# Performance work log

Measured on AMD Instinct MI355X. Metric: run time of the kernel, lower is better.

The kernel has to match this reference:

```python
import jax, jax.numpy as jnp
import numpy as np

N_IMG, BATCH, SEQ, D_IN, H = 32, 1024, 64, 16, 16


def setup_inputs() -> dict:
    key = jax.random.key(0)
    k1, k2, k3, k4, k5 = jax.random.split(key, 5)
    s = 1.0 / np.sqrt(H)  # torch nn.LSTM default init: U(-1/sqrt(H), 1/sqrt(H))
    return {
        "images": jax.random.normal(k1, (N_IMG, BATCH, SEQ, D_IN), jnp.float32),
        "w_ih": jax.random.uniform(k2, (4 * H, D_IN), jnp.float32, -s, s),
        "w_hh": jax.random.uniform(k3, (4 * H, H), jnp.float32, -s, s),
        "b_ih": jax.random.uniform(k4, (4 * H,), jnp.float32, -s, s),
        "b_hh": jax.random.uniform(k5, (4 * H,), jnp.float32, -s, s),
    }


def reference(images, w_ih, w_hh, b_ih, b_hh):
    # images: [N, B, S, D]. The torch module loops over N chunks, feeding each
    # [B, S, D] chunk through nn.LSTM while carrying (h, c) across chunks.
    # Equivalent: one continuous recurrence over N*S timesteps.
    n, b, s, d = images.shape
    h_dim = w_hh.shape[1]
    # time-major: [N*S, B, D]
    xs = images.transpose(0, 2, 1, 3).reshape(n * s, b, d)
    # precompute input projections for all timesteps (the only big GEMM)
    x_proj = jnp.einsum('tbd,gd->tbg', xs, w_ih) + (b_ih + b_hh)  # [T, B, 4H]

    def cell(carry, xp_t):
        h_prev, c_prev = carry
        gates = xp_t + h_prev @ w_hh.T  # [B, 4H]; torch gate order: i, f, g, o
        i, f, g, o = jnp.split(gates, 4, axis=-1)
        c = jax.nn.sigmoid(f) * c_prev + jax.nn.sigmoid(i) * jnp.tanh(g)
        h_new = jax.nn.sigmoid(o) * jnp.tanh(c)
        return (h_new, c), h_new

    h0 = jnp.zeros((b, h_dim), images.dtype)
    (_, _), outs = jax.lax.scan(cell, (h0, h0), x_proj)  # outs: [T, B, H]
    # torch stacks per-chunk outputs [B, S, H] along dim 0 -> [N, B, S, H]
    return outs.reshape(n, s, b, h_dim).transpose(0, 2, 1, 3)
```

## Files before the change

kernel.cpp:

```cpp
#include <hip/hip_runtime.h>

#define LOG2E      1.44269504088896340736f
#define TWO_LOG2E  2.88539008177792680472f

typedef float f2 __attribute__((ext_vector_type(2)));

__device__ __forceinline__ float frcp(float x)  { return __builtin_amdgcn_rcpf(x); }
__device__ __forceinline__ float fexp2(float x) { return __builtin_amdgcn_exp2f(x); }

__device__ __forceinline__ f2 pk_mul(f2 a, f2 b) {
    f2 d; asm("v_pk_mul_f32 %0, %1, %2" : "=v"(d) : "v"(a), "v"(b)); return d;
}
__device__ __forceinline__ f2 pk_fma(f2 a, f2 b, f2 c) {
    f2 d; asm("v_pk_fma_f32 %0, %1, %2, %3" : "=v"(d) : "v"(a), "v"(b), "v"(c)); return d;
}
__device__ __forceinline__ f2 pk_add(f2 a, f2 b) {
    f2 d; asm("v_pk_add_f32 %0, %1, %2" : "=v"(d) : "v"(a), "v"(b)); return d;
}

__device__ __forceinline__ void gload_lds16(const float* g, float* l) {
    auto gp = (const __attribute__((address_space(1))) float*)g;
    auto lp = (__attribute__((address_space(3))) float*)l;
    __builtin_amdgcn_global_load_lds(gp, lp, 16, 0, 0);
}


__global__ __launch_bounds__(256, 1)
void lstm_fused(const float* __restrict__ images,
                const float* __restrict__ w_ih,
                const float* __restrict__ w_hh,
                const float* __restrict__ b_ih,
                const float* __restrict__ b_hh,
                float* __restrict__ out)
{
    __shared__ float4 xlds[4][2][256];

    const int lane = threadIdx.x & 63;
    const int wid  = threadIdx.x >> 6;
    const int b    = (blockIdx.x << 2) + wid;
    const int a    = lane >> 4;
    const int j    = lane & 15;

    int rr1 = __builtin_amdgcn_update_dpp(0, j, 0x121, 0xF, 0xF, true);
    const int d_ror = (rr1 - j) & 15;

    int e16;
    { int pa = a, pb = a;
      asm volatile("s_nop 1\n\t"
                   "v_permlane16_swap_b32 %0, %1" : "+v"(pa), "+v"(pb));
      e16 = pa & 1; }
    int e32;
    { int pc = a, pd = a;
      asm volatile("s_nop 1\n\t"
                   "v_permlane32_swap_b32 %0, %1" : "+v"(pc), "+v"(pd));
      e32 = (pc < 2) ? 0 : 1; }

    const int m1 = ((a >> 1) == e32);
    const int m0 = ((a & 1) == e16);
    const int gate = m0 ? (m1 ? 1 : 2) : (m1 ? 0 : 3);
    const int r = gate * 16 + j;

    const float aa = (gate == 2) ? TWO_LOG2E : -LOG2E;
    const float mm = (gate == 2) ? -2.0f * TWO_LOG2E : 1.0f;
    const float dd = (gate == 2) ? TWO_LOG2E : 0.0f;

    float whh[16];
#pragma unroll
    for (int t = 0; t < 16; ++t)
        whh[t] = aa * w_hh[r * 16 + ((j + d_ror * t) & 15)];
    f2 wihp[8];
#pragma unroll
    for (int m = 0; m < 8; ++m) {
        f2 w; w.x = aa * w_ih[r * 16 + 2 * m]; w.y = aa * w_ih[r * 16 + 2 * m + 1];
        wihp[m] = w;
    }
    const float bias = aa * (b_ih[r] + b_hh[r]);

    float hv = 0.0f;
    float c  = 0.0f;
    float sv = 0.0f;

    const int bbase = b << 10;

#define PB(p) ((((p) >> 4) << 20) + bbase + (((((p) << 2)) & 63) << 4))

#define GLOAD_CHUNK(n) {                                                       \
        const float* gp_ = images + ((n) << 20) + bbase + (lane << 2);         \
        float4* lb_ = &xlds[wid][(n) & 1][0];                                  \
        gload_lds16(gp_ + 0,   (float*)(lb_ + 0));                             \
        gload_lds16(gp_ + 256, (float*)(lb_ + 64));                            \
        gload_lds16(gp_ + 512, (float*)(lb_ + 128));                           \
        gload_lds16(gp_ + 768, (float*)(lb_ + 192)); }

#define DSREAD(xv2, Qraw) {                                                    \
        int Q_ = (Qraw); if (Q_ > 511) Q_ = 511;                               \
        const float4* sp_ = &xlds[wid][(Q_ >> 4) & 1][(Q_ & 15) << 4];         \
        _Pragma("unroll")                                                      \
        for (int q = 0; q < 16; ++q) {                                         \
            float4 t_ = sp_[q];                                                \
            f2 lo_, hi_; lo_.x = t_.x; lo_.y = t_.y; hi_.x = t_.z; hi_.y = t_.w;\
            xv2[2*q] = lo_; xv2[2*q+1] = hi_;                                  \
        } }

#define PROJ(xpre, x2) {                                                       \
        _Pragma("unroll")                                                      \
        for (int u = 0; u < 4; ++u) {                                          \
            f2 A_ = pk_mul(wihp[0], x2[8*u+0]);                                \
            f2 B_ = pk_mul(wihp[1], x2[8*u+1]);                                \
            A_ = pk_fma(wihp[2], x2[8*u+2], A_);                               \
            B_ = pk_fma(wihp[3], x2[8*u+3], B_);                               \
            A_ = pk_fma(wihp[4], x2[8*u+4], A_);                               \
            B_ = pk_fma(wihp[5], x2[8*u+5], B_);                               \
            A_ = pk_fma(wihp[6], x2[8*u+6], A_);                               \
            B_ = pk_fma(wihp[7], x2[8*u+7], B_);                               \
            A_ = pk_add(A_, B_);                                               \
            xpre[u] = (bias + A_.x) + A_.y;                                    \
        } }

#define STEP(u, xpv) {                                                         \
        float p0 = (xpv), p1, p2, p3;                                          \
        asm volatile(                                                          \
          "s_nop 1\n\t"                                                        \
          "v_fmac_f32 %[q0], %[h], %[w0]\n\t"                                  \
          "v_mul_f32 %[q1], %[h], %[w1] row_ror:1 row_mask:0xf bank_mask:0xf\n\t" \
          "v_mul_f32 %[q2], %[h], %[w2] row_ror:2 row_mask:0xf bank_mask:0xf\n\t" \
          "v_mul_f32 %[q3], %[h], %[w3] row_ror:3 row_mask:0xf bank_mask:0xf\n\t" \
          "v_fmac_f32 %[q0], %[h], %[w4] row_ror:4 row_mask:0xf bank_mask:0xf\n\t" \
          "v_fmac_f32 %[q1], %[h], %[w5] row_ror:5 row_mask:0xf bank_mask:0xf\n\t" \
          "v_fmac_f32 %[q2], %[h], %[w6] row_ror:6 row_mask:0xf bank_mask:0xf\n\t" \
          "v_fmac_f32 %[q3], %[h], %[w7] row_ror:7 row_mask:0xf bank_mask:0xf\n\t" \
          "v_fmac_f32 %[q0], %[h], %[w8] row_ror:8 row_mask:0xf bank_mask:0xf\n\t" \
          "v_fmac_f32 %[q1], %[h], %[w9] row_ror:9 row_mask:0xf bank_mask:0xf\n\t" \
          "v_fmac_f32 %[q2], %[h], %[w10] row_ror:10 row_mask:0xf bank_mask:0xf\n\t" \
          "v_fmac_f32 %[q3], %[h], %[w11] row_ror:11 row_mask:0xf bank_mask:0xf\n\t" \
          "v_fmac_f32 %[q0], %[h], %[w12] row_ror:12 row_mask:0xf bank_mask:0xf\n\t" \
          "v_fmac_f32 %[q1], %[h], %[w13] row_ror:13 row_mask:0xf bank_mask:0xf\n\t" \
          "v_fmac_f32 %[q2], %[h], %[w14] row_ror:14 row_mask:0xf bank_mask:0xf\n\t" \
          "v_fmac_f32 %[q3], %[h], %[w15] row_ror:15 row_mask:0xf bank_mask:0xf"   \
          : [q0]"+v"(p0), [q1]"=&v"(p1), [q2]"=&v"(p2), [q3]"=&v"(p3)          \
          : [h]"v"(hv),                                                        \
            [w0]"v"(whh[0]),  [w1]"v"(whh[1]),  [w2]"v"(whh[2]),  [w3]"v"(whh[3]), \
            [w4]"v"(whh[4]),  [w5]"v"(whh[5]),  [w6]"v"(whh[6]),  [w7]"v"(whh[7]), \
            [w8]"v"(whh[8]),  [w9]"v"(whh[9]),  [w10]"v"(whh[10]),[w11]"v"(whh[11]),\
            [w12]"v"(whh[12]),[w13]"v"(whh[13]),[w14]"v"(whh[14]),[w15]"v"(whh[15]));\
        float arg = (p0 + p1) + (p2 + p3);                                     \
        float act = fmaf(mm, frcp(1.0f + fexp2(arg)), dd);                     \
        float qf, qg, qi, qo;                                                  \
        asm volatile(                                                          \
          "v_mov_b32 %[A], %[x]\n\t"                                           \
          "v_mov_b32 %[B], %[x]\n\t"                                           \
          "s_nop 1\n\t"                                                        \
          "v_permlane16_swap_b32 %[A], %[B]\n\t"                               \
          "v_mov_b32 %[C], %[A]\n\t"                                           \
          "v_mov_b32 %[D], %[B]\n\t"                                           \
          "v_permlane32_swap_b32 %[A], %[C]\n\t"                               \
          "v_permlane32_swap_b32 %[B], %[D]"                                   \
          : [A]"=&v"(qf), [B]"=&v"(qi), [C]"=&v"(qg), [D]"=&v"(qo)             \
          : [x]"v"(act));                                                      \
        c = fmaf(c, qf, qi * qg);                                              \
        float tc = fmaf(-2.0f, frcp(1.0f + fexp2(c)), 1.0f);                   \
        hv = qo * tc;                                                          \
        sv = (a == (u)) ? hv : sv;                                             \
    }

#define STORE(pb) out[(pb) + lane] = sv;

    f2    xvA[32], xvB[32];
    float xpre[4];

    GLOAD_CHUNK(0);
    GLOAD_CHUNK(1);
    DSREAD(xvA, 0);
    PROJ(xpre, xvA);
    DSREAD(xvB, 1);

#pragma unroll 1
    for (int P = 0; P < 512; P += 2) {
        {
            const int pb = PB(P);
            STEP(0, xpre[0]);
            STEP(1, xpre[1]);
            STEP(2, xpre[2]);
            STEP(3, xpre[3]);
            STORE(pb);
        }
        PROJ(xpre, xvB);
        DSREAD(xvA, P + 2);
        if ((P & 15) == 14 && P < 480)
            GLOAD_CHUNK((P >> 4) + 2);
        {
            const int pb = PB(P + 1);
            STEP(0, xpre[0]);
            STEP(1, xpre[1]);
            STEP(2, xpre[2]);
            STEP(3, xpre[3]);
            STORE(pb);
        }
        PROJ(xpre, xvA);
        DSREAD(xvB, P + 3);
    }

#undef STEP
#undef STORE
#undef PROJ
#undef DSREAD
#undef GLOAD_CHUNK
#undef PB
}

extern "C" void kernel_launch(void* const* d_in, const int* in_sizes, int n_in,
                              void* d_out, int out_size, void* d_ws, size_t ws_size,
                              hipStream_t stream)
{
    const float* images = (const float*)d_in[0];
    const float* w_ih   = (const float*)d_in[1];
    const float* w_hh   = (const float*)d_in[2];
    const float* b_ih   = (const float*)d_in[3];
    const float* b_hh   = (const float*)d_in[4];
    float* outp         = (float*)d_out;

    lstm_fused<<<dim3(256), dim3(256), 0, stream>>>(images, w_ih, w_hh, b_ih, b_hh, outp);
}
```

Baseline: 324.1 us.

## Hand-schedule LDS reads with explicit waitcnt and shorten the tanh chain

Result: faster. 292.6 us (-9.7%).

```diff
diff --git a/kernel.cpp b/kernel.cpp
--- a/kernel.cpp
+++ b/kernel.cpp
@@ -17,6 +17,8 @@
 __device__ __forceinline__ f2 pk_add(f2 a, f2 b) {
     f2 d; asm("v_pk_add_f32 %0, %1, %2" : "=v"(d) : "v"(a), "v"(b)); return d;
 }
+__device__ __forceinline__ f2 f2lo(float4 v) { f2 r; r.x = v.x; r.y = v.y; return r; }
+__device__ __forceinline__ f2 f2hi(float4 v) { f2 r; r.x = v.z; r.y = v.w; return r; }
 
 __device__ __forceinline__ void gload_lds16(const float* g, float* l) {
     auto gp = (const __attribute__((address_space(1))) float*)g;
@@ -76,6 +78,8 @@
     }
     const float bias = aa * (b_ih[r] + b_hh[r]);
 
+    const bool su0 = (a == 0), su1 = (a == 1), su2 = (a == 2), su3 = (a == 3);
+
     float hv = 0.0f;
     float c  = 0.0f;
     float sv = 0.0f;
@@ -92,35 +96,37 @@
         gload_lds16(gp_ + 512, (float*)(lb_ + 128));                           \
         gload_lds16(gp_ + 768, (float*)(lb_ + 192)); }
 
-#define DSREAD(xv2, Qraw) {                                                    \
+#define DSREADV(xv, Qraw) {                                                    \
         int Q_ = (Qraw); if (Q_ > 511) Q_ = 511;                               \
-        const float4* sp_ = &xlds[wid][(Q_ >> 4) & 1][(Q_ & 15) << 4];         \
+        auto lp_ = (const __attribute__((address_space(3))) float4*)           \
+                   &xlds[wid][(Q_ >> 4) & 1][(Q_ & 15) << 4];                  \
         _Pragma("unroll")                                                      \
-        for (int q = 0; q < 16; ++q) {                                         \
-            float4 t_ = sp_[q];                                                \
-            f2 lo_, hi_; lo_.x = t_.x; lo_.y = t_.y; hi_.x = t_.z; hi_.y = t_.w;\
-            xv2[2*q] = lo_; xv2[2*q+1] = hi_;                                  \
-        } }
-
-#define PROJ(xpre, x2) {                                                       \
+        for (int q = 0; q < 16; ++q)                                           \
+            asm volatile("ds_read_b128 %0, %1 offset:%2"                       \
+                : "=v"(xv[q]) : "v"(lp_), "i"(q * 16) : "memory");             \
+    }
+
+#define WAIT_LGKM() { asm volatile("s_waitcnt lgkmcnt(0)" ::: "memory");       \
+                      __builtin_amdgcn_sched_barrier(0); }
+
+#define PROJ(xpre, xv) {                                                       \
         _Pragma("unroll")                                                      \
         for (int u = 0; u < 4; ++u) {                                          \
-            f2 A_ = pk_mul(wihp[0], x2[8*u+0]);                                \
-            f2 B_ = pk_mul(wihp[1], x2[8*u+1]);                                \
-            A_ = pk_fma(wihp[2], x2[8*u+2], A_);                               \
-            B_ = pk_fma(wihp[3], x2[8*u+3], B_);                               \
-            A_ = pk_fma(wihp[4], x2[8*u+4], A_);                               \
-            B_ = pk_fma(wihp[5], x2[8*u+5], B_);                               \
-            A_ = pk_fma(wihp[6], x2[8*u+6], A_);                               \
-            B_ = pk_fma(wihp[7], x2[8*u+7], B_);                               \
+            f2 A_ = pk_mul(wihp[0], f2lo(xv[4*u+0]));                          \
+            f2 B_ = pk_mul(wihp[1], f2hi(xv[4*u+0]));                          \
+            A_ = pk_fma(wihp[2], f2lo(xv[4*u+1]), A_);                         \
+            B_ = pk_fma(wihp[3], f2hi(xv[4*u+1]), B_);                         \
+            A_ = pk_fma(wihp[4], f2lo(xv[4*u+2]), A_);                         \
+            B_ = pk_fma(wihp[5], f2hi(xv[4*u+2]), B_);                         \
+            A_ = pk_fma(wihp[6], f2lo(xv[4*u+3]), A_);                         \
+            B_ = pk_fma(wihp[7], f2hi(xv[4*u+3]), B_);                         \
             A_ = pk_add(A_, B_);                                               \
             xpre[u] = (bias + A_.x) + A_.y;                                    \
         } }
 
-#define STEP(u, xpv) {                                                         \
+#define STEP(SU, xpv) {                                                        \
         float p0 = (xpv), p1, p2, p3;                                          \
-        asm volatile(                                                          \
-          "s_nop 1\n\t"                                                        \
+        asm("s_nop 1\n\t"                                                      \
           "v_fmac_f32 %[q0], %[h], %[w0]\n\t"                                  \
           "v_mul_f32 %[q1], %[h], %[w1] row_ror:1 row_mask:0xf bank_mask:0xf\n\t" \
           "v_mul_f32 %[q2], %[h], %[w2] row_ror:2 row_mask:0xf bank_mask:0xf\n\t" \
@@ -146,8 +152,7 @@
         float arg = (p0 + p1) + (p2 + p3);                                     \
         float act = fmaf(mm, frcp(1.0f + fexp2(arg)), dd);                     \
         float qf, qg, qi, qo;                                                  \
-        asm volatile(                                                          \
-          "v_mov_b32 %[A], %[x]\n\t"                                           \
+        asm("v_mov_b32 %[A], %[x]\n\t"                                         \
           "v_mov_b32 %[B], %[x]\n\t"                                           \
           "s_nop 1\n\t"                                                        \
           "v_permlane16_swap_b32 %[A], %[B]\n\t"                               \
@@ -157,53 +162,61 @@
           "v_permlane32_swap_b32 %[B], %[D]"                                   \
           : [A]"=&v"(qf), [B]"=&v"(qi), [C]"=&v"(qg), [D]"=&v"(qo)             \
           : [x]"v"(act));                                                      \
-        c = fmaf(c, qf, qi * qg);                                              \
-        float tc = fmaf(-2.0f, frcp(1.0f + fexp2(c)), 1.0f);                   \
-        hv = qo * tc;                                                          \
-        sv = (a == (u)) ? hv : sv;                                             \
+        float ig = qi * qg;                                                    \
+        float qo2 = qo + qo;                                                   \
+        c = fmaf(c, qf, ig);                                                   \
+        float rr = frcp(1.0f + fexp2(c));                                      \
+        hv = fmaf(-qo2, rr, qo);                                               \
+        sv = (SU) ? hv : sv;                                                   \
     }
 
 #define STORE(pb) out[(pb) + lane] = sv;
 
-    f2    xvA[32], xvB[32];
-    float xpre[4];
+    float4 xvA[16], xvB[16];
+    float  xpre0[4], xpre1[4];
 
     GLOAD_CHUNK(0);
     GLOAD_CHUNK(1);
-    DSREAD(xvA, 0);
-    PROJ(xpre, xvA);
-    DSREAD(xvB, 1);
+    asm volatile("s_waitcnt vmcnt(0)" ::: "memory");
+    DSREADV(xvA, 0);
+    WAIT_LGKM();
+    PROJ(xpre0, xvA);
+    DSREADV(xvB, 1);
 
 #pragma unroll 1
     for (int P = 0; P < 512; P += 2) {
+        DSREADV(xvA, P + 2);
         {
             const int pb = PB(P);
-            STEP(0, xpre[0]);
-            STEP(1, xpre[1]);
-            STEP(2, xpre[2]);
-            STEP(3, xpre[3]);
+            STEP(su0, xpre0[0]);
+            STEP(su1, xpre0[1]);
+            STEP(su2, xpre0[2]);
+            STEP(su3, xpre0[3]);
             STORE(pb);
         }
-        PROJ(xpre, xvB);
-        DSREAD(xvA, P + 2);
+        if ((P & 15) == 8)
+            asm volatile("s_waitcnt vmcnt(0)" ::: "memory");
+        WAIT_LGKM();
+        PROJ(xpre1, xvB);
+        {
+            const int pb = PB(P + 1);
+            STEP(su0, xpre1[0]);
+            STEP(su1, xpre1[1]);
+            STEP(su2, xpre1[2]);
+            STEP(su3, xpre1[3]);
+            STORE(pb);
+        }
+        DSREADV(xvB, P + 3);
+        PROJ(xpre0, xvA);
         if ((P & 15) == 14 && P < 480)
             GLOAD_CHUNK((P >> 4) + 2);
-        {
-            const int pb = PB(P + 1);
-            STEP(0, xpre[0]);
-            STEP(1, xpre[1]);
-            STEP(2, xpre[2]);
-            STEP(3, xpre[3]);
-            STORE(pb);
-        }
-        PROJ(xpre, xvA);
-        DSREAD(xvB, P + 3);
     }
 
 #undef STEP
 #undef STORE
 #undef PROJ
-#undef DSREAD
+#undef WAIT_LGKM
+#undef DSREADV
 #undef GLOAD_CHUNK
 #undef PB
 }
```
